# Kernel tuning notes

Measured on AMD Instinct MI355X. Metric: run time of the kernel, lower is better.

Reference implementation:

```python
import jax, jax.numpy as jnp
import numpy as np

B, T, V, H = 256, 512, 64, 256
IN = 2 * V + 1  # values + masks + delta_t = 129


def setup_inputs() -> dict:
    key = jax.random.key(0)
    ks = jax.random.split(key, 8)
    # sorted positive times with some entries zeroed (ragged padding -> t_exist False)
    t = jnp.sort(jax.random.uniform(ks[0], (B, T)), axis=1)
    keep = jax.random.uniform(ks[1], (B, T)) < 0.9
    times_in = jnp.where(keep, t, 0.0).astype(jnp.float32)
    data_in = jax.random.normal(ks[2], (B, T, V), dtype=jnp.float32)
    mask_in = (jax.random.uniform(ks[3], (B, T, V)) < 0.8).astype(jnp.float32)
    s = 1.0 / np.sqrt(H).astype(np.float32)
    W_ih = jax.random.uniform(ks[4], (3 * H, IN), minval=-s, maxval=s, dtype=jnp.float32)
    W_hh = jax.random.uniform(ks[5], (3 * H, H), minval=-s, maxval=s, dtype=jnp.float32)
    b_ih = jax.random.uniform(ks[6], (3 * H,), minval=-s, maxval=s, dtype=jnp.float32)
    b_hh = jax.random.uniform(ks[7], (3 * H,), minval=-s, maxval=s, dtype=jnp.float32)
    return {"times_in": times_in, "data_in": data_in, "mask_in": mask_in,
            "W_ih": W_ih, "W_hh": W_hh, "b_ih": b_ih, "b_hh": b_hh}


def reference(times_in, data_in, mask_in, W_ih, W_hh, b_ih, b_hh):
    b = times_in.shape[0]
    # delta_ts: times[:,1:] - times[:,:-1], padded with zero at the end
    delta = jnp.concatenate(
        [times_in[:, 1:] - times_in[:, :-1],
         jnp.zeros((b, 1), times_in.dtype)], axis=1)  # [B,T]
    # input_series = cat(values, masks, delta_t) -> [B,T,2V+1]
    x = jnp.concatenate([data_in, mask_in, delta[..., None]], axis=-1)
    t_exist = times_in > 0  # [B,T]
    h0 = jnp.zeros((b, W_hh.shape[1]), x.dtype)

    xs = (jnp.swapaxes(x, 0, 1), jnp.swapaxes(t_exist, 0, 1))  # time-major

    def step(h, inp):
        xt, m = inp  # xt: [B,IN], m: [B]
        gx = xt @ W_ih.T + b_ih  # [B,3H]
        gh = h @ W_hh.T + b_hh   # [B,3H]
        xr, xz, xn = jnp.split(gx, 3, axis=-1)
        hr, hz, hn = jnp.split(gh, 3, axis=-1)
        r = jax.nn.sigmoid(xr + hr)
        z = jax.nn.sigmoid(xz + hz)
        n = jnp.tanh(xn + r * hn)
        h_new = (1.0 - z) * n + z * h
        h = jnp.where(m[:, None], h_new, h)  # masked state carry
        return h, None

    h_final, _ = jax.lax.scan(step, h0, xs)
    return h_final
```

## Files before the change

kernel.cpp:

```cpp
#include <hip/hip_runtime.h>

#define Bn 256
#define Tn 512
#define Vn 64
#define Hn 256
#define INn 129
#define Cc 8
#define NCH (Tn / Cc)
#define WU 68
#define WSZ (768 * WU)
#define GX_OFF (262144)
#define GX_BYTES ((size_t)Bn * Tn * 768 * 2)
#define AST 168
#define CST 264

typedef __fp16 half2_t __attribute__((ext_vector_type(2)));
typedef __fp16 half8_t __attribute__((ext_vector_type(8)));
typedef float f32x4 __attribute__((ext_vector_type(4)));

static __device__ __forceinline__ unsigned int cvt2(float a, float b) {
  return __builtin_bit_cast(unsigned int, __builtin_amdgcn_cvt_pkrtz(a, b));
}

static __device__ __forceinline__ float dot2(unsigned int w, unsigned int x, float acc) {
#if __has_builtin(__builtin_amdgcn_fdot2)
  return __builtin_amdgcn_fdot2(__builtin_bit_cast(half2_t, w),
                                __builtin_bit_cast(half2_t, x), acc, false);
#else
  half2_t a = __builtin_bit_cast(half2_t, w);
  half2_t b = __builtin_bit_cast(half2_t, x);
  return acc + (float)a.x * (float)b.x + (float)a.y * (float)b.y;
#endif
}

static __device__ __forceinline__ float pair_sum(float v) {
#if __has_builtin(__builtin_amdgcn_update_dpp)
  int x = __builtin_amdgcn_update_dpp(0, __builtin_bit_cast(int, v), 0xB1, 0xF, 0xF, true);
  return v + __builtin_bit_cast(float, x);
#else
  int j = __builtin_amdgcn_ds_swizzle(__builtin_bit_cast(int, v), 0x041F);
  return v + __builtin_bit_cast(float, j);
#endif
}

static __device__ __forceinline__ float quad_sum(float v) {
#if __has_builtin(__builtin_amdgcn_update_dpp)
  int x = __builtin_amdgcn_update_dpp(0, __builtin_bit_cast(int, v), 0xB1, 0xF, 0xF, true);
  v += __builtin_bit_cast(float, x);
  int y = __builtin_amdgcn_update_dpp(0, __builtin_bit_cast(int, v), 0x4E, 0xF, 0xF, true);
  v += __builtin_bit_cast(float, y);
  return v;
#else
  int j = __builtin_amdgcn_ds_swizzle(__builtin_bit_cast(int, v), 0x041F);
  v += __builtin_bit_cast(float, j);
  j = __builtin_amdgcn_ds_swizzle(__builtin_bit_cast(int, v), 0x081F);
  v += __builtin_bit_cast(float, j);
  return v;
#endif
}

static __device__ __forceinline__ float fast_exp2(float x) {
#if __has_builtin(__builtin_amdgcn_exp2f)
  return __builtin_amdgcn_exp2f(x);
#else
  return exp2f(x);
#endif
}
static __device__ __forceinline__ float fast_rcp(float x) {
#if __has_builtin(__builtin_amdgcn_rcpf)
  return __builtin_amdgcn_rcpf(x);
#else
  return 1.f / x;
#endif
}
static __device__ __forceinline__ float sigmoid_f(float x) {
  return fast_rcp(1.f + fast_exp2(-1.44269504f * x));
}
static __device__ __forceinline__ float tanh_f(float x) {
  return 1.f - 2.f * fast_rcp(1.f + fast_exp2(2.88539008f * x));
}

__global__ void convert_wih(const float* __restrict__ W_ih, unsigned int* __restrict__ w16) {
  int idx = blockIdx.x * 256 + threadIdx.x;
  if (idx >= WSZ) return;
  int j = idx / WU, c = idx - j * WU;
  int col = 2 * c;
  float f0 = (col < INn) ? W_ih[(size_t)j * INn + col] : 0.f;
  float f1 = (col + 1 < INn) ? W_ih[(size_t)j * INn + col + 1] : 0.f;
  w16[idx] = cvt2(f0, f1);
}

__global__ __launch_bounds__(256, 4)
void gx_gemm(const float* __restrict__ times_in, const float* __restrict__ data_in,
             const float* __restrict__ mask_in, const unsigned int* __restrict__ w16,
             const float* __restrict__ b_ih, __fp16* __restrict__ gx) {
  __shared__ __align__(16) char raw[64 * CST * 2];
  __fp16* xa = (__fp16*)raw;
  __fp16* ct = (__fp16*)raw;

  const int tid = threadIdx.x;
  const int bt = blockIdx.x;
  const int b = bt >> 3, tc = bt & 7;
  const int t0 = tc * 64;
  const int n0 = blockIdx.y * 256;

  {
    int r = tid >> 2, s = tid & 3;
    const float* src = (s < 2)
        ? data_in + ((size_t)b * Tn + t0 + r) * Vn + s * 32
        : mask_in + ((size_t)b * Tn + t0 + r) * Vn + (s - 2) * 32;
    unsigned int* dst = (unsigned int*)(xa + r * AST) + s * 16;
#pragma unroll
    for (int i = 0; i < 8; ++i) {
      float4 v = ((const float4*)src)[i];
      dst[2 * i] = cvt2(v.x, v.y);
      dst[2 * i + 1] = cvt2(v.z, v.w);
    }
  }
  if (tid < 64) {
    int g = t0 + tid;
    float tcur = times_in[(size_t)b * Tn + g];
    float d = (g < Tn - 1) ? times_in[(size_t)b * Tn + g + 1] - tcur : 0.f;
    unsigned int* p = (unsigned int*)(xa + tid * AST + 128);
    p[0] = cvt2(d, 0.f);
#pragma unroll
    for (int i = 1; i < 20; ++i) p[i] = 0u;
  }
  __syncthreads();

  const int w = tid >> 6, lane = tid & 63;
  const int m = lane & 15, q = lane >> 4;
  const int nw = n0 + w * 64;

  f32x4 acc[4][4];
#pragma unroll
  for (int i = 0; i < 4; ++i)
#pragma unroll
    for (int j = 0; j < 4; ++j) acc[i][j] = f32x4{0.f, 0.f, 0.f, 0.f};

#pragma unroll
  for (int kt = 0; kt < 5; ++kt) {
    const int k0 = kt * 32 + q * 8;
    half8_t bf[4], af[4];
#pragma unroll
    for (int nt = 0; nt < 4; ++nt) {
      int n = nw + nt * 16 + m;
      uint4 bv = *(const uint4*)(w16 + (size_t)n * WU + (k0 >> 1));
      bf[nt] = __builtin_bit_cast(half8_t, bv);
    }
#pragma unroll
    for (int mt = 0; mt < 4; ++mt) {
      uint4 av = *(const uint4*)(xa + (mt * 16 + m) * AST + k0);
      af[mt] = __builtin_bit_cast(half8_t, av);
    }
#pragma unroll
    for (int mt = 0; mt < 4; ++mt)
#pragma unroll
      for (int nt = 0; nt < 4; ++nt)
        acc[mt][nt] = __builtin_amdgcn_mfma_f32_16x16x32_f16(af[mt], bf[nt], acc[mt][nt], 0, 0, 0);
  }

  float bias[4];
#pragma unroll
  for (int nt = 0; nt < 4; ++nt) bias[nt] = b_ih[nw + nt * 16 + m];

  __syncthreads();
#pragma unroll
  for (int mt = 0; mt < 4; ++mt)
#pragma unroll
    for (int nt = 0; nt < 4; ++nt)
#pragma unroll
      for (int r = 0; r < 4; ++r)
        ct[(mt * 16 + q * 4 + r) * CST + w * 64 + nt * 16 + m] =
            (__fp16)(acc[mt][nt][r] + bias[nt]);
  __syncthreads();

  {
    const int tt = tid >> 2, qq = tid & 3;
    const uint4* src = (const uint4*)(ct + tt * CST) + qq * 8;
    uint4* dst = (uint4*)(gx + ((size_t)b * Tn + t0 + tt) * 768 + n0) + qq * 8;
#pragma unroll
    for (int i = 0; i < 8; ++i) dst[i] = src[i];
  }
}

#define DOT4(hv, base)                                                                     \
  sr = dot2(whr[(base) + 0], hv.x, sr); sz = dot2(whz[(base) + 0], hv.x, sz);              \
  shn = dot2(whn[(base) + 0], hv.x, shn);                                                  \
  sr = dot2(whr[(base) + 1], hv.y, sr); sz = dot2(whz[(base) + 1], hv.y, sz);              \
  shn = dot2(whn[(base) + 1], hv.y, shn);                                                  \
  sr = dot2(whr[(base) + 2], hv.z, sr); sz = dot2(whz[(base) + 2], hv.z, sz);              \
  shn = dot2(whn[(base) + 2], hv.z, shn);                                                  \
  sr = dot2(whr[(base) + 3], hv.w, sr); sz = dot2(whz[(base) + 3], hv.w, sz);              \
  shn = dot2(whn[(base) + 3], hv.w, shn);

__global__ __launch_bounds__(1024, 1)
void gru_scan4(const float* __restrict__ times_in, const float* __restrict__ W_hh,
               const float* __restrict__ b_hh, const __fp16* __restrict__ gx,
               float* __restrict__ out) {
  __shared__ __align__(16) __fp16 h_buf[2 * Hn];
  __shared__ __align__(16) float t_lds[Tn];

  const int tid = threadIdx.x;
  const int b = blockIdx.x;
  const int jg = tid >> 2;
  const int ks = tid & 3;

  if (tid < Tn) t_lds[tid] = times_in[(size_t)b * Tn + tid];

  unsigned int whr[32], whz[32], whn[32];
  {
    const float* w0 = W_hh + (size_t)jg * Hn + ks * 64;
    const float* w1 = W_hh + (size_t)(jg + 256) * Hn + ks * 64;
    const float* w2 = W_hh + (size_t)(jg + 512) * Hn + ks * 64;
#pragma unroll
    for (int c = 0; c < 32; ++c) {
      whr[c] = cvt2(w0[2 * c], w0[2 * c + 1]);
      whz[c] = cvt2(w1[2 * c], w1[2 * c + 1]);
      whn[c] = cvt2(w2[2 * c], w2[2 * c + 1]);
    }
  }
  const float brh = b_hh[jg];
  const float bzh = b_hh[jg + 256];
  const float bhn = b_hh[jg + 512];

  if (tid < 2 * Hn) h_buf[tid] = (__fp16)0.f;
  __syncthreads();

  const __fp16* gxb = gx + (size_t)b * Tn * 768;
  float hcur = 0.f;

  float gr = (float)gxb[jg], gz = (float)gxb[256 + jg], gn = (float)gxb[512 + jg];
  float mt = t_lds[0];

#pragma unroll 1
  for (int t = 0; t < Tn; ++t) {
    const int tn = (t + 1 < Tn) ? (t + 1) : (Tn - 1);
    const __fp16* p = gxb + (size_t)tn * 768;
    __fp16 pr = p[jg], pz = p[256 + jg], pn = p[512 + jg];
    float mtn = t_lds[tn];

    const int cur = t & 1;
    const uint4* hb = (const uint4*)(h_buf + cur * Hn) + ks * 8;

    float sr = 0.f, sz = 0.f, shn = 0.f;
    {
      uint4 h0 = hb[0], h1 = hb[1], h2 = hb[2], h3 = hb[3];
      DOT4(h0, 0) DOT4(h1, 4) DOT4(h2, 8) DOT4(h3, 12)
    }
    {
      uint4 h4 = hb[4], h5 = hb[5], h6 = hb[6], h7 = hb[7];
      DOT4(h4, 16) DOT4(h5, 20) DOT4(h6, 24) DOT4(h7, 28)
    }

    sr = quad_sum(sr);
    sz = quad_sum(sz);
    shn = quad_sum(shn);

    float r = sigmoid_f(gr + sr + brh);
    float z = sigmoid_f(gz + sz + bzh);
    float n = tanh_f(gn + r * (shn + bhn));
    float hN = (1.f - z) * n + z * hcur;
    hcur = (mt > 0.f) ? hN : hcur;

    if (ks == 0) h_buf[(cur ^ 1) * Hn + jg] = (__fp16)hcur;
    __syncthreads();

    gr = (float)pr; gz = (float)pz; gn = (float)pn; mt = mtn;
  }

  if (ks == 0) out[(size_t)b * Hn + jg] = hcur;
}

template <bool USE_WS>
static __device__ __forceinline__ void phaseA_pass(int col, const unsigned int* __restrict__ w16,
                                                   const float* __restrict__ W_ih,
                                                   const unsigned int* x_lds, float* a) {
  const uint4* wp = (const uint4*)(w16) + (size_t)col * (WU / 4);
  const float* wf = W_ih + (size_t)col * INn;
#pragma unroll 2
  for (int kp = 0; kp < 8; ++kp) {
    uint4 wa, wb;
    if constexpr (USE_WS) {
      wa = wp[2 * kp];
      wb = wp[2 * kp + 1];
    } else {
      const float* f = wf + 16 * kp;
      wa.x = cvt2(f[0], f[1]);   wa.y = cvt2(f[2], f[3]);
      wa.z = cvt2(f[4], f[5]);   wa.w = cvt2(f[6], f[7]);
      wb.x = cvt2(f[8], f[9]);   wb.y = cvt2(f[10], f[11]);
      wb.z = cvt2(f[12], f[13]); wb.w = cvt2(f[14], f[15]);
    }
#pragma unroll
    for (int t = 0; t < Cc; ++t) {
      const uint4* xp = (const uint4*)&x_lds[t * WU + kp * 8];
      uint4 xa = xp[0], xb = xp[1];
      a[t] = dot2(wa.x, xa.x, a[t]);
      a[t] = dot2(wa.y, xa.y, a[t]);
      a[t] = dot2(wa.z, xa.z, a[t]);
      a[t] = dot2(wa.w, xa.w, a[t]);
      a[t] = dot2(wb.x, xb.x, a[t]);
      a[t] = dot2(wb.y, xb.y, a[t]);
      a[t] = dot2(wb.z, xb.z, a[t]);
      a[t] = dot2(wb.w, xb.w, a[t]);
    }
  }
  uint4 wt;
  if constexpr (USE_WS) {
    wt = wp[16];
  } else {
    wt.x = cvt2(wf[128], 0.f); wt.y = 0u; wt.z = 0u; wt.w = 0u;
  }
#pragma unroll
  for (int t = 0; t < Cc; ++t) {
    uint4 xt = *(const uint4*)&x_lds[t * WU + 64];
    a[t] = dot2(wt.x, xt.x, a[t]);
    a[t] = dot2(wt.y, xt.y, a[t]);
  }
}

template <bool USE_WS>
__global__ __launch_bounds__(512, 2)
void gru_scan_fb(const float* __restrict__ times_in, const float* __restrict__ data_in,
                 const float* __restrict__ mask_in, const unsigned int* __restrict__ w16,
                 const float* __restrict__ W_ih, const float* __restrict__ W_hh,
                 const float* __restrict__ b_ih, const float* __restrict__ b_hh,
                 float* __restrict__ out) {
  __shared__ __align__(16) float gx_lds[Cc * 768];
  __shared__ __align__(16) unsigned int x_lds[Cc * WU];
  __shared__ __align__(16) __fp16 h_buf[2 * Hn];
  __shared__ __align__(16) float t_lds[Tn];

  const int tid = threadIdx.x;
  const int b = blockIdx.x;
  const int jg = tid >> 1;
  const int ks = tid & 1;

  t_lds[tid] = times_in[(size_t)b * Tn + tid];

  unsigned int whr[64], whz[64], whn[64];
  {
    const float* w0 = W_hh + (size_t)jg * Hn + ks * 128;
    const float* w1 = W_hh + (size_t)(jg + 256) * Hn + ks * 128;
    const float* w2 = W_hh + (size_t)(jg + 512) * Hn + ks * 128;
#pragma unroll
    for (int c = 0; c < 64; ++c) {
      whr[c] = cvt2(w0[2 * c], w0[2 * c + 1]);
      whz[c] = cvt2(w1[2 * c], w1[2 * c + 1]);
      whn[c] = cvt2(w2[2 * c], w2[2 * c + 1]);
    }
  }
  const float brh = b_hh[jg];
  const float bzh = b_hh[jg + 256];
  const float bhn = b_hh[jg + 512];
  const float bi1 = b_ih[tid];
  const float bi2 = (tid < 256) ? b_ih[512 + tid] : 0.f;

  h_buf[tid] = (__fp16)0.f;
  __syncthreads();

  float hcur = 0.f;
  int cur = 0;
#pragma unroll 1
  for (int ch = 0; ch < NCH; ++ch) {
    const int t0 = ch * Cc;
    {
      int t = tid >> 6;
      int c = tid & 63;
      const float* src = (c < 32)
          ? data_in + ((size_t)b * Tn + t0 + t) * Vn + 2 * c
          : mask_in + ((size_t)b * Tn + t0 + t) * Vn + 2 * (c - 32);
      float2 v = *(const float2*)src;
      x_lds[t * WU + c] = cvt2(v.x, v.y);
      if (tid < Cc) {
        int g = t0 + tid;
        float d = (g < Tn - 1) ? (t_lds[g + 1] - t_lds[g]) : 0.f;
        uint4 tl;
        tl.x = cvt2(d, 0.f); tl.y = 0u; tl.z = 0u; tl.w = 0u;
        *(uint4*)&x_lds[tid * WU + 64] = tl;
      }
    }
    __syncthreads();
    {
      float a[Cc];
#pragma unroll
      for (int t = 0; t < Cc; ++t) a[t] = bi1;
      phaseA_pass<USE_WS>(tid, w16, W_ih, x_lds, a);
#pragma unroll
      for (int t = 0; t < Cc; ++t) gx_lds[t * 768 + tid] = a[t];
      if (tid < 256) {
#pragma unroll
        for (int t = 0; t < Cc; ++t) a[t] = bi2;
        phaseA_pass<USE_WS>(512 + tid, w16, W_ih, x_lds, a);
#pragma unroll
        for (int t = 0; t < Cc; ++t) gx_lds[t * 768 + 512 + tid] = a[t];
      }
    }
    __syncthreads();
    for (int tt = 0; tt < Cc; ++tt) {
      float sr = 0.f, sz = 0.f, shn = 0.f;
      const uint4* hb = (const uint4*)(h_buf + cur * Hn + ks * 128);
#pragma unroll
      for (int c = 0; c < 16; ++c) {
        uint4 hv = hb[c];
        sr = dot2(whr[4 * c + 0], hv.x, sr);
        sz = dot2(whz[4 * c + 0], hv.x, sz);
        shn = dot2(whn[4 * c + 0], hv.x, shn);
        sr = dot2(whr[4 * c + 1], hv.y, sr);
        sz = dot2(whz[4 * c + 1], hv.y, sz);
        shn = dot2(whn[4 * c + 1], hv.y, shn);
        sr = dot2(whr[4 * c + 2], hv.z, sr);
        sz = dot2(whz[4 * c + 2], hv.z, sz);
        shn = dot2(whn[4 * c + 2], hv.z, shn);
        sr = dot2(whr[4 * c + 3], hv.w, sr);
        sz = dot2(whz[4 * c + 3], hv.w, sz);
        shn = dot2(whn[4 * c + 3], hv.w, shn);
      }
      float gxr = gx_lds[tt * 768 + jg];
      float gxz = gx_lds[tt * 768 + 256 + jg];
      float gxn = gx_lds[tt * 768 + 512 + jg];
      sr = pair_sum(sr);
      sz = pair_sum(sz);
      shn = pair_sum(shn);
      float r = sigmoid_f(gxr + sr + brh);
      float z = sigmoid_f(gxz + sz + bzh);
      float n = tanh_f(gxn + r * (shn + bhn));
      float hN = (1.f - z) * n + z * hcur;
      hcur = (t_lds[t0 + tt] > 0.f) ? hN : hcur;
      if (ks == 0) h_buf[(cur ^ 1) * Hn + jg] = (__fp16)hcur;
      __syncthreads();
      cur ^= 1;
    }
  }
  if (ks == 0) out[(size_t)b * Hn + jg] = hcur;
}

extern "C" void kernel_launch(void* const* d_in, const int* in_sizes, int n_in,
                              void* d_out, int out_size, void* d_ws, size_t ws_size,
                              hipStream_t stream) {
  const float* times_in = (const float*)d_in[0];
  const float* data_in = (const float*)d_in[1];
  const float* mask_in = (const float*)d_in[2];
  const float* W_ih = (const float*)d_in[3];
  const float* W_hh = (const float*)d_in[4];
  const float* b_ih = (const float*)d_in[5];
  const float* b_hh = (const float*)d_in[6];
  float* out = (float*)d_out;

  unsigned int* w16 = (unsigned int*)d_ws;
  __fp16* gx = (__fp16*)((char*)d_ws + GX_OFF);

  if (ws_size >= GX_OFF + GX_BYTES) {
    hipLaunchKernelGGL(convert_wih, dim3((WSZ + 255) / 256), dim3(256), 0, stream, W_ih, w16);
    hipLaunchKernelGGL(gx_gemm, dim3(2048, 3), dim3(256), 0, stream,
                       times_in, data_in, mask_in, w16, b_ih, gx);
    hipLaunchKernelGGL(gru_scan4, dim3(Bn), dim3(1024), 0, stream,
                       times_in, W_hh, b_hh, gx, out);
  } else if (ws_size >= (size_t)WSZ * 4) {
    hipLaunchKernelGGL(convert_wih, dim3((WSZ + 255) / 256), dim3(256), 0, stream, W_ih, w16);
    hipLaunchKernelGGL((gru_scan_fb<true>), dim3(Bn), dim3(512), 0, stream,
                       times_in, data_in, mask_in, w16, W_ih, W_hh, b_ih, b_hh, out);
  } else {
    hipLaunchKernelGGL((gru_scan_fb<false>), dim3(Bn), dim3(512), 0, stream,
                       times_in, data_in, mask_in, (const unsigned int*)nullptr, W_ih, W_hh,
                       b_ih, b_hh, out);
  }
}
```

Baseline: 858.5 us.

## Compute GRU recurrent matvec with MFMA and fold hidden r/z biases into gx

Replaces the per-thread packed-fp16 dot-product scan with a 512-thread kernel. W_hh is held in registers as MFMA A-fragments and h_t is broadcast as the B operand of 16x16x32 f16 MFMAs, which removes the cross-lane quad reductions. The r and z hidden biases are folded into the gx GEMM bias. The gx and time loads are no longer prefetched one step ahead, so global load latency now sits on the serial critical path. The MFMA also computes 16 identical columns, of which only one is used.

```diff
diff --git a/kernel.cpp b/kernel.cpp
--- a/kernel.cpp
+++ b/kernel.cpp
@@ -43,22 +43,6 @@
 #endif
 }
 
-static __device__ __forceinline__ float quad_sum(float v) {
-#if __has_builtin(__builtin_amdgcn_update_dpp)
-  int x = __builtin_amdgcn_update_dpp(0, __builtin_bit_cast(int, v), 0xB1, 0xF, 0xF, true);
-  v += __builtin_bit_cast(float, x);
-  int y = __builtin_amdgcn_update_dpp(0, __builtin_bit_cast(int, v), 0x4E, 0xF, 0xF, true);
-  v += __builtin_bit_cast(float, y);
-  return v;
-#else
-  int j = __builtin_amdgcn_ds_swizzle(__builtin_bit_cast(int, v), 0x041F);
-  v += __builtin_bit_cast(float, j);
-  j = __builtin_amdgcn_ds_swizzle(__builtin_bit_cast(int, v), 0x081F);
-  v += __builtin_bit_cast(float, j);
-  return v;
-#endif
-}
-
 static __device__ __forceinline__ float fast_exp2(float x) {
 #if __has_builtin(__builtin_amdgcn_exp2f)
   return __builtin_amdgcn_exp2f(x);
@@ -78,6 +62,11 @@
 }
 static __device__ __forceinline__ float tanh_f(float x) {
   return 1.f - 2.f * fast_rcp(1.f + fast_exp2(2.88539008f * x));
+}
+
+static __device__ __forceinline__ float half_at(uint2 u, int r) {
+  half2_t p = __builtin_bit_cast(half2_t, (r < 2) ? u.x : u.y);
+  return (float)p[r & 1];
 }
 
 __global__ void convert_wih(const float* __restrict__ W_ih, unsigned int* __restrict__ w16) {
@@ -93,7 +82,8 @@
 __global__ __launch_bounds__(256, 4)
 void gx_gemm(const float* __restrict__ times_in, const float* __restrict__ data_in,
              const float* __restrict__ mask_in, const unsigned int* __restrict__ w16,
-             const float* __restrict__ b_ih, __fp16* __restrict__ gx) {
+             const float* __restrict__ b_ih, const float* __restrict__ b_hh,
+             __fp16* __restrict__ gx) {
   __shared__ __align__(16) char raw[64 * CST * 2];
   __fp16* xa = (__fp16*)raw;
   __fp16* ct = (__fp16*)raw;
@@ -162,7 +152,10 @@
 
   float bias[4];
 #pragma unroll
-  for (int nt = 0; nt < 4; ++nt) bias[nt] = b_ih[nw + nt * 16 + m];
+  for (int nt = 0; nt < 4; ++nt) {
+    int n = nw + nt * 16 + m;
+    bias[nt] = b_ih[n] + ((n < 512) ? b_hh[n] : 0.f);
+  }
 
   __syncthreads();
 #pragma unroll
@@ -184,92 +177,111 @@
   }
 }
 
-#define DOT4(hv, base)                                                                     \
-  sr = dot2(whr[(base) + 0], hv.x, sr); sz = dot2(whz[(base) + 0], hv.x, sz);              \
-  shn = dot2(whn[(base) + 0], hv.x, shn);                                                  \
-  sr = dot2(whr[(base) + 1], hv.y, sr); sz = dot2(whz[(base) + 1], hv.y, sz);              \
-  shn = dot2(whn[(base) + 1], hv.y, shn);                                                  \
-  sr = dot2(whr[(base) + 2], hv.z, sr); sz = dot2(whz[(base) + 2], hv.z, sz);              \
-  shn = dot2(whn[(base) + 2], hv.z, shn);                                                  \
-  sr = dot2(whr[(base) + 3], hv.w, sr); sz = dot2(whz[(base) + 3], hv.w, sz);              \
-  shn = dot2(whn[(base) + 3], hv.w, shn);
-
-__global__ __launch_bounds__(1024, 1)
-void gru_scan4(const float* __restrict__ times_in, const float* __restrict__ W_hh,
+__global__ __launch_bounds__(512, 2)
+void gru_scan5(const float* __restrict__ times_in, const float* __restrict__ W_hh,
                const float* __restrict__ b_hh, const __fp16* __restrict__ gx,
                float* __restrict__ out) {
-  __shared__ __align__(16) __fp16 h_buf[2 * Hn];
-  __shared__ __align__(16) float t_lds[Tn];
+  __shared__ __align__(16) __fp16 h_buf[2][Hn];
 
   const int tid = threadIdx.x;
   const int b = blockIdx.x;
-  const int jg = tid >> 2;
-  const int ks = tid & 3;
-
-  if (tid < Tn) t_lds[tid] = times_in[(size_t)b * Tn + tid];
-
-  unsigned int whr[32], whz[32], whn[32];
-  {
-    const float* w0 = W_hh + (size_t)jg * Hn + ks * 64;
-    const float* w1 = W_hh + (size_t)(jg + 256) * Hn + ks * 64;
-    const float* w2 = W_hh + (size_t)(jg + 512) * Hn + ks * 64;
-#pragma unroll
-    for (int c = 0; c < 32; ++c) {
-      whr[c] = cvt2(w0[2 * c], w0[2 * c + 1]);
-      whz[c] = cvt2(w1[2 * c], w1[2 * c + 1]);
-      whn[c] = cvt2(w2[2 * c], w2[2 * c + 1]);
-    }
-  }
-  const float brh = b_hh[jg];
-  const float bzh = b_hh[jg + 256];
-  const float bhn = b_hh[jg + 512];
-
-  if (tid < 2 * Hn) h_buf[tid] = (__fp16)0.f;
+  const int w = tid >> 6;
+  const int lane = tid & 63;
+  const int m = lane & 15;
+  const int q = lane >> 4;
+  const int rbase = 32 * w;
+
+  uint4 afr[3][2][8];
+#pragma unroll
+  for (int g = 0; g < 3; ++g)
+#pragma unroll
+    for (int t2 = 0; t2 < 2; ++t2) {
+      const float* wrow = W_hh + (size_t)(g * 256 + rbase + 16 * t2 + m) * Hn + q * 8;
+#pragma unroll
+      for (int kc = 0; kc < 8; ++kc) {
+        float4 v0 = *(const float4*)(wrow + kc * 32);
+        float4 v1 = *(const float4*)(wrow + kc * 32 + 4);
+        afr[g][t2][kc] = make_uint4(cvt2(v0.x, v0.y), cvt2(v0.z, v0.w),
+                                    cvt2(v1.x, v1.y), cvt2(v1.z, v1.w));
+      }
+    }
+
+  float bhn[2][4];
+#pragma unroll
+  for (int t2 = 0; t2 < 2; ++t2) {
+    float4 bv = *(const float4*)(b_hh + 512 + rbase + 16 * t2 + q * 4);
+    bhn[t2][0] = bv.x; bhn[t2][1] = bv.y; bhn[t2][2] = bv.z; bhn[t2][3] = bv.w;
+  }
+
+  if (tid < Hn) h_buf[0][tid] = (__fp16)0.f;
   __syncthreads();
 
   const __fp16* gxb = gx + (size_t)b * Tn * 768;
-  float hcur = 0.f;
-
-  float gr = (float)gxb[jg], gz = (float)gxb[256 + jg], gn = (float)gxb[512 + jg];
-  float mt = t_lds[0];
+  float hc[2][4] = {{0.f, 0.f, 0.f, 0.f}, {0.f, 0.f, 0.f, 0.f}};
 
 #pragma unroll 1
   for (int t = 0; t < Tn; ++t) {
-    const int tn = (t + 1 < Tn) ? (t + 1) : (Tn - 1);
-    const __fp16* p = gxb + (size_t)tn * 768;
-    __fp16 pr = p[jg], pz = p[256 + jg], pn = p[512 + jg];
-    float mtn = t_lds[tn];
-
     const int cur = t & 1;
-    const uint4* hb = (const uint4*)(h_buf + cur * Hn) + ks * 8;
-
-    float sr = 0.f, sz = 0.f, shn = 0.f;
-    {
-      uint4 h0 = hb[0], h1 = hb[1], h2 = hb[2], h3 = hb[3];
-      DOT4(h0, 0) DOT4(h1, 4) DOT4(h2, 8) DOT4(h3, 12)
-    }
-    {
-      uint4 h4 = hb[4], h5 = hb[5], h6 = hb[6], h7 = hb[7];
-      DOT4(h4, 16) DOT4(h5, 20) DOT4(h6, 24) DOT4(h7, 28)
-    }
-
-    sr = quad_sum(sr);
-    sz = quad_sum(sz);
-    shn = quad_sum(shn);
-
-    float r = sigmoid_f(gr + sr + brh);
-    float z = sigmoid_f(gz + sz + bzh);
-    float n = tanh_f(gn + r * (shn + bhn));
-    float hN = (1.f - z) * n + z * hcur;
-    hcur = (mt > 0.f) ? hN : hcur;
-
-    if (ks == 0) h_buf[(cur ^ 1) * Hn + jg] = (__fp16)hcur;
+
+    const __fp16* gpt = gxb + (size_t)t * 768 + rbase + q * 4;
+    uint2 gxr[2], gxz[2], gxn[2];
+#pragma unroll
+    for (int t2 = 0; t2 < 2; ++t2) {
+      gxr[t2] = *(const uint2*)(gpt + 16 * t2);
+      gxz[t2] = *(const uint2*)(gpt + 256 + 16 * t2);
+      gxn[t2] = *(const uint2*)(gpt + 512 + 16 * t2);
+    }
+    const float mt = times_in[(size_t)b * Tn + t];
+
+    f32x4 acc[3][2];
+#pragma unroll
+    for (int g = 0; g < 3; ++g)
+#pragma unroll
+      for (int t2 = 0; t2 < 2; ++t2) acc[g][t2] = f32x4{0.f, 0.f, 0.f, 0.f};
+
+    const uint4* hb = (const uint4*)(&h_buf[cur][0]);
+#pragma unroll
+    for (int kc = 0; kc < 8; ++kc) {
+      half8_t bfrag = __builtin_bit_cast(half8_t, hb[kc * 4 + q]);
+#pragma unroll
+      for (int g = 0; g < 3; ++g)
+#pragma unroll
+        for (int t2 = 0; t2 < 2; ++t2)
+          acc[g][t2] = __builtin_amdgcn_mfma_f32_16x16x32_f16(
+              __builtin_bit_cast(half8_t, afr[g][t2][kc]), bfrag, acc[g][t2], 0, 0, 0);
+    }
+
+#pragma unroll
+    for (int t2 = 0; t2 < 2; ++t2)
+#pragma unroll
+      for (int r = 0; r < 4; ++r) {
+        float rg = sigmoid_f(half_at(gxr[t2], r) + acc[0][t2][r]);
+        float zg = sigmoid_f(half_at(gxz[t2], r) + acc[1][t2][r]);
+        float ng = tanh_f(half_at(gxn[t2], r) + rg * (acc[2][t2][r] + bhn[t2][r]));
+        float hN = (1.f - zg) * ng + zg * hc[t2][r];
+        hc[t2][r] = (mt > 0.f) ? hN : hc[t2][r];
+      }
+
+    if (m == 0) {
+#pragma unroll
+      for (int t2 = 0; t2 < 2; ++t2) {
+        uint2 hp;
+        hp.x = cvt2(hc[t2][0], hc[t2][1]);
+        hp.y = cvt2(hc[t2][2], hc[t2][3]);
+        *(uint2*)&h_buf[cur ^ 1][rbase + 16 * t2 + q * 4] = hp;
+      }
+    }
     __syncthreads();
-
-    gr = (float)pr; gz = (float)pz; gn = (float)pn; mt = mtn;
-  }
-
-  if (ks == 0) out[(size_t)b * Hn + jg] = hcur;
+  }
+
+  if (m == 0) {
+#pragma unroll
+    for (int t2 = 0; t2 < 2; ++t2) {
+      float4 o;
+      o.x = hc[t2][0]; o.y = hc[t2][1]; o.z = hc[t2][2]; o.w = hc[t2][3];
+      *(float4*)(out + (size_t)b * Hn + rbase + 16 * t2 + q * 4) = o;
+    }
+  }
 }
 
 template <bool USE_WS>
@@ -453,8 +465,8 @@
   if (ws_size >= GX_OFF + GX_BYTES) {
     hipLaunchKernelGGL(convert_wih, dim3((WSZ + 255) / 256), dim3(256), 0, stream, W_ih, w16);
     hipLaunchKernelGGL(gx_gemm, dim3(2048, 3), dim3(256), 0, stream,
-                       times_in, data_in, mask_in, w16, b_ih, gx);
-    hipLaunchKernelGGL(gru_scan4, dim3(Bn), dim3(1024), 0, stream,
+                       times_in, data_in, mask_in, w16, b_ih, b_hh, gx);
+    hipLaunchKernelGGL(gru_scan5, dim3(Bn), dim3(512), 0, stream,
                        times_in, W_hh, b_hh, gx, out);
   } else if (ws_size >= (size_t)WSZ * 4) {
     hipLaunchKernelGGL(convert_wih, dim3((WSZ + 255) / 256), dim3(256), 0, stream, W_ih, w16);
```

New measurement: 1.519 ms. 1.77x slower.
